# Performance work log

Hardware: AMD Instinct MI355X
Metric: run time of the kernel (lower is better)

Reference implementation:

```python
import jax, jax.numpy as jnp
import numpy as np

HEADS = 8
DIM_HEAD = 64

def setup_inputs() -> dict:
    key = jax.random.key(0)
    k1, k2 = jax.random.split(key)
    x = jax.random.normal(k1, (4, 2048, 512), dtype=jnp.float32)
    W_qkv = jax.random.normal(k2, (512, 3 * HEADS * DIM_HEAD), dtype=jnp.float32) * (512 ** -0.5)
    return {"x": x, "W_qkv": W_qkv}

def reference(x, W_qkv):
    b, n, _ = x.shape
    h, d = HEADS, DIM_HEAD
    scale = d ** -0.5
    qkv = x @ W_qkv                                   # [b, n, 3*h*d]
    q, k, v = jnp.split(qkv, 3, axis=-1)
    # 'b n (h d) -> b h n d'
    q = q.reshape(b, n, h, d).transpose(0, 2, 1, 3)
    k = k.reshape(b, n, h, d).transpose(0, 2, 1, 3)
    v = v.reshape(b, n, h, d).transpose(0, 2, 1, 3)
    scores = jnp.einsum('bhid,bhjd->bhij', q, k) * scale
    attn_w = jax.nn.softmax(scores, axis=-1)
    out = jnp.einsum('bhij,bhjd->bhid', attn_w, v)
    # 'b h i d -> b i (h d)'
    return out.transpose(0, 2, 1, 3).reshape(b, n, h * d)
```

## Files before the change

kernel.cpp:

```cpp
#include <hip/hip_runtime.h>

#define BATCH 4
#define NSEQ  2048
#define DMODEL 512
#define NHEAD 8
#define DHEAD 64
#define NQKV  1536

typedef __bf16 bf16x8 __attribute__((ext_vector_type(8)));
typedef __bf16 bf16x4 __attribute__((ext_vector_type(4)));
typedef float  f32x4  __attribute__((ext_vector_type(4)));
typedef short  s16x4  __attribute__((ext_vector_type(4)));

__device__ inline void async16(const __bf16* g, __bf16* l) {
    __builtin_amdgcn_global_load_lds(
        (const __attribute__((address_space(1))) void*)g,
        (__attribute__((address_space(3))) void*)l, 16, 0, 0);
}

__device__ inline bf16x8 cvt8(const float* __restrict__ p) {
    float4 a = *(const float4*)p;
    float4 b = *(const float4*)(p + 4);
    bf16x8 r;
    r[0] = (__bf16)a.x; r[1] = (__bf16)a.y; r[2] = (__bf16)a.z; r[3] = (__bf16)a.w;
    r[4] = (__bf16)b.x; r[5] = (__bf16)b.y; r[6] = (__bf16)b.z; r[7] = (__bf16)b.w;
    return r;
}

__device__ inline f32x4 mfma_pv(s16x4 a, s16x4 b, f32x4 c) {
#if !defined(__HIP_DEVICE_COMPILE__)
    (void)a; (void)b;
    return c;
#elif __has_builtin(__builtin_amdgcn_mfma_f32_16x16x16bf16_1k)
    return __builtin_amdgcn_mfma_f32_16x16x16bf16_1k(a, b, c, 0, 0, 0);
#else
    bf16x4 a4 = __builtin_bit_cast(bf16x4, a);
    bf16x4 b4 = __builtin_bit_cast(bf16x4, b);
    bf16x8 a8 = {}, b8 = {};
    for (int i = 0; i < 4; ++i) { a8[i] = a4[i]; b8[i] = b4[i]; }
    return __builtin_amdgcn_mfma_f32_16x16x32_bf16(a8, b8, c, 0, 0, 0);
#endif
}

#define QSCALE 0.18033688011112042f

__global__ __launch_bounds__(256) void prep_kernel(
    const float* __restrict__ W, __bf16* __restrict__ Wt,
    const float* __restrict__ x, __bf16* __restrict__ xb) {
    const int tid = threadIdx.x;
    const int bi = blockIdx.x;
    if (bi >= 192) {
        int g = ((bi - 192) * 256 + tid) * 8;
        bf16x8 r = cvt8(&x[g]);
        *(bf16x8*)&xb[g] = r;
        return;
    }
    __shared__ __bf16 t[64][65];
    const int n0 = (bi % 24) * 64, k0 = (bi / 24) * 64;
    const int cr = tid >> 4;
    const int cc = (tid & 15) * 4;
    for (int p = 0; p < 4; ++p) {
        int r = p * 16 + cr;
        float4 v = *(const float4*)&W[(size_t)(k0 + r) * NQKV + n0 + cc];
        t[r][cc + 0] = (__bf16)v.x; t[r][cc + 1] = (__bf16)v.y;
        t[r][cc + 2] = (__bf16)v.z; t[r][cc + 3] = (__bf16)v.w;
    }
    __syncthreads();
    for (int p = 0; p < 4; ++p) {
        int r = p * 16 + cr;
        bf16x4 o = {t[cc + 0][r], t[cc + 1][r], t[cc + 2][r], t[cc + 3][r]};
        *(bf16x4*)&Wt[(size_t)(n0 + r) * DMODEL + k0 + cc] = o;
    }
}

__global__ __launch_bounds__(512) void qkv_gemm_kernel(
    const __bf16* __restrict__ xb, const __bf16* __restrict__ Wt,
    __bf16* __restrict__ Qw, __bf16* __restrict__ Kw, __bf16* __restrict__ Vw) {
    __shared__ __align__(16) char smem[49152];
    __bf16* Al = (__bf16*)smem;
    __bf16* Bl = Al + 16384;
    __bf16* T  = (__bf16*)smem;

    const int tid  = threadIdx.x;
    const int w    = tid >> 6;
    const int lane = tid & 63;
    const int quad = lane >> 4;
    const int l15  = lane & 15;
    const int wm   = w >> 1, wn = w & 1;
    const int m0 = blockIdx.x * 256;
    const int n0 = blockIdx.y * 128;
    const int segrow = lane >> 3;
    const int sc = (lane & 7) ^ segrow;

    f32x4 acc[4][4];
    for (int i = 0; i < 4; ++i)
        for (int j = 0; j < 4; ++j)
            acc[i][j] = (f32x4){0.f, 0.f, 0.f, 0.f};

    for (int kt = 0; kt < 8; ++kt) {
        const int k0 = kt * 64;
        for (int i = 0; i < 2; ++i) {
            int seg = w * 2 + i;
            int row = seg * 8 + segrow;
            async16(&Wt[(size_t)(n0 + row) * DMODEL + k0 + sc * 8], &Bl[seg * 512]);
        }
        for (int i = 0; i < 4; ++i) {
            int seg = w * 4 + i;
            int row = seg * 8 + segrow;
            async16(&xb[(size_t)(m0 + row) * DMODEL + k0 + sc * 8], &Al[seg * 512]);
        }
        __syncthreads();
        for (int kc = 0; kc < 2; ++kc) {
            bf16x8 af[4], bfr[4];
            for (int mb = 0; mb < 4; ++mb) {
                int row = wm * 64 + mb * 16 + l15;
                af[mb] = *(const bf16x8*)&Al[(row >> 3) * 512 +
                    ((row & 7) * 8 + ((kc * 4 + quad) ^ (row & 7))) * 8];
            }
            for (int nb = 0; nb < 4; ++nb) {
                int row = wn * 64 + nb * 16 + l15;
                bfr[nb] = *(const bf16x8*)&Bl[row * 64 + (((kc * 4 + quad) ^ (l15 & 7)) * 8)];
            }
            for (int mb = 0; mb < 4; ++mb)
                for (int nb = 0; nb < 4; ++nb)
                    acc[mb][nb] = __builtin_amdgcn_mfma_f32_16x16x32_bf16(
                        af[mb], bfr[nb], acc[mb][nb], 0, 0, 0);
        }
        __syncthreads();
    }

    const int which = n0 >> 9;
    const int bb  = m0 >> 11;
    const int nq0 = m0 & 2047;

    for (int ph = 0; ph < 2; ++ph) {
        if (which <= 1) {
            if ((wm >> 1) == ph)
                for (int mb = 0; mb < 4; ++mb)
                    for (int nb = 0; nb < 4; ++nb)
                        for (int r = 0; r < 4; ++r) {
                            int ml = (wm & 1) * 64 + mb * 16 + quad * 4 + r;
                            int nl = wn * 64 + nb * 16 + l15;
                            float a = acc[mb][nb][r];
                            if (which == 0) a *= QSCALE;
                            T[ml * 136 + nl] = (__bf16)a;
                        }
            __syncthreads();
            __bf16* dst = which ? Kw : Qw;
            const int h0 = (n0 & 511) >> 6;
            const int region = tid >> 8;
            const int bh = bb * NHEAD + h0 + region;
            __bf16* base = dst + ((size_t)bh * NSEQ + nq0 + ph * 128) * DHEAD;
            for (int i = 0; i < 4; ++i) {
                int chunk = (tid & 255) + i * 256;
                int f = chunk * 8;
                int ml = f >> 6, dd = f & 63;
                bf16x8 v = *(const bf16x8*)&T[ml * 136 + region * 64 + dd];
                *(bf16x8*)&base[ml * 64 + dd] = v;
            }
        } else {
            if ((wm >> 1) == ph)
                for (int mb = 0; mb < 4; ++mb)
                    for (int nb = 0; nb < 4; ++nb) {
                        int nl = wn * 64 + nb * 16 + l15;
                        int mlb = (wm & 1) * 64 + mb * 16 + quad * 4;
                        bf16x4 v = {(__bf16)acc[mb][nb][0], (__bf16)acc[mb][nb][1],
                                    (__bf16)acc[mb][nb][2], (__bf16)acc[mb][nb][3]};
                        *(bf16x4*)&T[nl * 136 + mlb] = v;
                    }
            __syncthreads();
            const int hv0 = ((n0 - 1024) & 511) >> 6;
            for (int i = 0; i < 4; ++i) {
                int gc = i * 512 + tid;
                int row = gc >> 4, ch = gc & 15;
                bf16x8 v = *(const bf16x8*)&T[row * 136 + ch * 8];
                int bh = bb * NHEAD + hv0 + (row >> 6);
                int dd = row & 63;
                *(bf16x8*)&Vw[((size_t)bh * DHEAD + dd) * NSEQ + nq0 + ph * 128 + ch * 8] = v;
            }
        }
        __syncthreads();
    }
}

__global__ __launch_bounds__(512) void attn_kernel(
    const __bf16* __restrict__ Qw, const __bf16* __restrict__ Kw,
    const __bf16* __restrict__ Vw, float* __restrict__ out) {
    __shared__ __align__(16) char smem[65536];
    float* Of = (float*)smem;

    const int tid  = threadIdx.x;
    const int w    = tid >> 6;
    const int wg   = w & 3;
    const int half = w >> 2;
    const int lane = tid & 63;
    const int quad = lane >> 4;
    const int l15  = lane & 15;
    const int bh = blockIdx.y;
    const int bb = bh >> 3, h = bh & 7;
    const int q0 = blockIdx.x * 128 + wg * 32;
    const int segrow = lane >> 3;
    const int sc = (lane & 7) ^ segrow;

    __bf16* HB = (__bf16*)smem + half * 16384;

    const __bf16* Qh = Qw + (size_t)bh * NSEQ * DHEAD;
    const __bf16* Kh = Kw + (size_t)bh * NSEQ * DHEAD;
    const __bf16* Vh = Vw + (size_t)bh * DHEAD * NSEQ;

    bf16x8 qf[2][2];
#pragma unroll
    for (int qb = 0; qb < 2; ++qb)
#pragma unroll
        for (int kc = 0; kc < 2; ++kc)
            qf[qb][kc] = *(const bf16x8*)&Qh[(size_t)(q0 + qb * 16 + l15) * DHEAD + kc * 32 + quad * 8];

    int offk[2][4], offv[4][4];
#pragma unroll
    for (int kc = 0; kc < 2; ++kc)
#pragma unroll
        for (int kb = 0; kb < 4; ++kb)
            offk[kc][kb] = (kb * 16 + l15) * 64 + (((kc * 4 + quad) ^ (l15 & 7)) * 8);
#pragma unroll
    for (int kb = 0; kb < 4; ++kb)
#pragma unroll
        for (int db = 0; db < 4; ++db) {
            int d = db * 16 + l15;
            int g = kb * 2 + (quad >> 1);
            offv[kb][db] = (d >> 3) * 512 + (d & 7) * 64 +
                           ((g ^ (d & 7)) * 8) + (quad & 1) * 4;
        }

    const f32x4 fzero = (f32x4){0.f, 0.f, 0.f, 0.f};

    f32x4 O[4][2];
    float l_st[2] = {0.f, 0.f};
#pragma unroll
    for (int db = 0; db < 4; ++db)
#pragma unroll
        for (int qb = 0; qb < 2; ++qb)
            O[db][qb] = fzero;

    auto stage = [&](int it, int b) {
        const int k0 = (half * 16 + it) * 64;
        __bf16* KL = HB + b * 8192;
        __bf16* VL = KL + 4096;
        for (int i = 0; i < 2; ++i) {
            int seg = wg * 2 + i;
            int row = seg * 8 + segrow;
            async16(&Kh[(size_t)(k0 + row) * DHEAD + sc * 8], &KL[seg * 512]);
            async16(&Vh[(size_t)row * NSEQ + k0 + sc * 8], &VL[seg * 512]);
        }
    };

    stage(0, 0);
    for (int it = 0; it < 16; ++it) {
        __syncthreads();
        if (it < 15) stage(it + 1, (it + 1) & 1);
        const __bf16* Kb = HB + (it & 1) * 8192;
        const __bf16* Vb = Kb + 4096;

        f32x4 s[4][2];
#pragma unroll
        for (int kc = 0; kc < 2; ++kc) {
            bf16x8 ak[4];
#pragma unroll
            for (int kb = 0; kb < 4; ++kb)
                ak[kb] = *(const bf16x8*)&Kb[offk[kc][kb]];
#pragma unroll
            for (int kb = 0; kb < 4; ++kb)
#pragma unroll
                for (int qb = 0; qb < 2; ++qb)
                    s[kb][qb] = __builtin_amdgcn_mfma_f32_16x16x32_bf16(
                        ak[kb], qf[qb][kc], kc == 0 ? fzero : s[kb][qb], 0, 0, 0);
        }

        s16x4 pb[4][2];
#pragma unroll
        for (int qb = 0; qb < 2; ++qb) {
            float rsum = 0.f;
#pragma unroll
            for (int kb = 0; kb < 4; ++kb) {
                bf16x4 t;
#pragma unroll
                for (int r = 0; r < 4; ++r) {
                    float p = __builtin_amdgcn_exp2f(s[kb][qb][r]);
                    rsum += p;
                    t[r] = (__bf16)p;
                }
                pb[kb][qb] = __builtin_bit_cast(s16x4, t);
            }
            l_st[qb] += rsum;
        }

#pragma unroll
        for (int kb = 0; kb < 4; ++kb) {
            s16x4 av[4];
#pragma unroll
            for (int db = 0; db < 4; ++db)
                av[db] = *(const s16x4*)&Vb[offv[kb][db]];
#pragma unroll
            for (int db = 0; db < 4; ++db)
#pragma unroll
                for (int qb = 0; qb < 2; ++qb)
                    O[db][qb] = mfma_pv(av[db], pb[kb][qb], O[db][qb]);
        }
    }

    for (int qb = 0; qb < 2; ++qb) {
        l_st[qb] += __shfl_xor(l_st[qb], 16);
        l_st[qb] += __shfl_xor(l_st[qb], 32);
    }

    __syncthreads();
    if (half == 0) {
        for (int qb = 0; qb < 2; ++qb) {
            int q = wg * 32 + qb * 16 + l15;
            for (int db = 0; db < 4; ++db)
                *(f32x4*)&Of[q * 68 + db * 16 + quad * 4] = O[db][qb];
            if (quad == 0) Of[q * 68 + 64] = l_st[qb];
        }
    }
    __syncthreads();
    if (half == 1) {
        for (int qb = 0; qb < 2; ++qb) {
            int q = wg * 32 + qb * 16 + l15;
            float inv = 1.f / (l_st[qb] + Of[q * 68 + 64]);
            for (int db = 0; db < 4; ++db) {
                f32x4 v = *(const f32x4*)&Of[q * 68 + db * 16 + quad * 4];
                v = (v + O[db][qb]) * inv;
                *(f32x4*)&Of[q * 68 + db * 16 + quad * 4] = v;
            }
        }
    }
    __syncthreads();
    const int nqb = blockIdx.x * 128;
    for (int i = 0; i < 4; ++i) {
        int gc = i * 512 + tid;
        int row = gc >> 4, ch = gc & 15;
        f32x4 v = *(const f32x4*)&Of[row * 68 + ch * 4];
        *(f32x4*)&out[((size_t)(bb * NSEQ + nqb + row)) * DMODEL + h * DHEAD + ch * 4] = v;
    }
}

extern "C" void kernel_launch(void* const* d_in, const int* in_sizes, int n_in,
                              void* d_out, int out_size, void* d_ws, size_t ws_size,
                              hipStream_t stream) {
    const float* x = (const float*)d_in[0];
    const float* W = (const float*)d_in[1];
    float* out = (float*)d_out;

    __bf16* wsp = (__bf16*)d_ws;
    __bf16* Wt = wsp;
    __bf16* Qw = Wt + 786432;
    __bf16* Kw = Qw + 4194304;
    __bf16* Vw = Kw + 4194304;
    __bf16* xb = Vw + 4194304;

    prep_kernel<<<2240, 256, 0, stream>>>(W, Wt, x, xb);
    qkv_gemm_kernel<<<dim3(32, 12), 512, 0, stream>>>(xb, Wt, Qw, Kw, Vw);
    attn_kernel<<<dim3(16, 32), 512, 0, stream>>>(Qw, Kw, Vw, out);
}
```

Baseline: 132.9 us.

## Halve attention query tile and drop K/V double buffering to raise occupancy

The attention kernel now handles 64 queries per block instead of 128, with one 16-row query tile per wave. The grid doubles to 1024 blocks and shared memory is halved to 32KB by switching from double-buffered to single-buffered K/V staging, with a second barrier before each refill. Launch bounds request higher occupancy so more blocks can sit on each CU. In exchange, each K/V tile is reused by half as many queries, so global K/V traffic doubles, and the load of the next tile no longer overlaps with compute inside a block.

```diff
diff --git a/kernel.cpp b/kernel.cpp
--- a/kernel.cpp
+++ b/kernel.cpp
@@ -183,10 +183,10 @@
     }
 }
 
-__global__ __launch_bounds__(512) void attn_kernel(
+__global__ __launch_bounds__(512, 8) void attn_kernel(
     const __bf16* __restrict__ Qw, const __bf16* __restrict__ Kw,
     const __bf16* __restrict__ Vw, float* __restrict__ out) {
-    __shared__ __align__(16) char smem[65536];
+    __shared__ __align__(16) char smem[32768];
     float* Of = (float*)smem;
 
     const int tid  = threadIdx.x;
@@ -198,22 +198,20 @@
     const int l15  = lane & 15;
     const int bh = blockIdx.y;
     const int bb = bh >> 3, h = bh & 7;
-    const int q0 = blockIdx.x * 128 + wg * 32;
+    const int q0 = blockIdx.x * 64 + wg * 16;
     const int segrow = lane >> 3;
     const int sc = (lane & 7) ^ segrow;
 
-    __bf16* HB = (__bf16*)smem + half * 16384;
+    __bf16* HB = (__bf16*)smem + half * 8192;
 
     const __bf16* Qh = Qw + (size_t)bh * NSEQ * DHEAD;
     const __bf16* Kh = Kw + (size_t)bh * NSEQ * DHEAD;
     const __bf16* Vh = Vw + (size_t)bh * DHEAD * NSEQ;
 
-    bf16x8 qf[2][2];
-#pragma unroll
-    for (int qb = 0; qb < 2; ++qb)
-#pragma unroll
-        for (int kc = 0; kc < 2; ++kc)
-            qf[qb][kc] = *(const bf16x8*)&Qh[(size_t)(q0 + qb * 16 + l15) * DHEAD + kc * 32 + quad * 8];
+    bf16x8 qf[2];
+#pragma unroll
+    for (int kc = 0; kc < 2; ++kc)
+        qf[kc] = *(const bf16x8*)&Qh[(size_t)(q0 + l15) * DHEAD + kc * 32 + quad * 8];
 
     int offk[2][4], offv[4][4];
 #pragma unroll
@@ -233,18 +231,16 @@
 
     const f32x4 fzero = (f32x4){0.f, 0.f, 0.f, 0.f};
 
-    f32x4 O[4][2];
-    float l_st[2] = {0.f, 0.f};
+    f32x4 O[4];
+    float l_st = 0.f;
 #pragma unroll
     for (int db = 0; db < 4; ++db)
-#pragma unroll
-        for (int qb = 0; qb < 2; ++qb)
-            O[db][qb] = fzero;
-
-    auto stage = [&](int it, int b) {
+        O[db] = fzero;
+
+    auto stage = [&](int it) {
         const int k0 = (half * 16 + it) * 64;
-        __bf16* KL = HB + b * 8192;
-        __bf16* VL = KL + 4096;
+        __bf16* KL = HB;
+        __bf16* VL = HB + 4096;
         for (int i = 0; i < 2; ++i) {
             int seg = wg * 2 + i;
             int row = seg * 8 + segrow;
@@ -253,14 +249,13 @@
         }
     };
 
-    stage(0, 0);
+    stage(0);
     for (int it = 0; it < 16; ++it) {
         __syncthreads();
-        if (it < 15) stage(it + 1, (it + 1) & 1);
-        const __bf16* Kb = HB + (it & 1) * 8192;
-        const __bf16* Vb = Kb + 4096;
-
-        f32x4 s[4][2];
+        const __bf16* Kb = HB;
+        const __bf16* Vb = HB + 4096;
+
+        f32x4 s[4];
 #pragma unroll
         for (int kc = 0; kc < 2; ++kc) {
             bf16x8 ak[4];
@@ -269,28 +264,25 @@
                 ak[kb] = *(const bf16x8*)&Kb[offk[kc][kb]];
 #pragma unroll
             for (int kb = 0; kb < 4; ++kb)
-#pragma unroll
-                for (int qb = 0; qb < 2; ++qb)
-                    s[kb][qb] = __builtin_amdgcn_mfma_f32_16x16x32_bf16(
-                        ak[kb], qf[qb][kc], kc == 0 ? fzero : s[kb][qb], 0, 0, 0);
-        }
-
-        s16x4 pb[4][2];
-#pragma unroll
-        for (int qb = 0; qb < 2; ++qb) {
+                s[kb] = __builtin_amdgcn_mfma_f32_16x16x32_bf16(
+                    ak[kb], qf[kc], kc == 0 ? fzero : s[kb], 0, 0, 0);
+        }
+
+        s16x4 pb[4];
+        {
             float rsum = 0.f;
 #pragma unroll
             for (int kb = 0; kb < 4; ++kb) {
                 bf16x4 t;
 #pragma unroll
                 for (int r = 0; r < 4; ++r) {
-                    float p = __builtin_amdgcn_exp2f(s[kb][qb][r]);
+                    float p = __builtin_amdgcn_exp2f(s[kb][r]);
                     rsum += p;
                     t[r] = (__bf16)p;
                 }
-                pb[kb][qb] = __builtin_bit_cast(s16x4, t);
-            }
-            l_st[qb] += rsum;
+                pb[kb] = __builtin_bit_cast(s16x4, t);
+            }
+            l_st += rsum;
         }
 
 #pragma unroll
@@ -301,41 +293,37 @@
                 av[db] = *(const s16x4*)&Vb[offv[kb][db]];
 #pragma unroll
             for (int db = 0; db < 4; ++db)
-#pragma unroll
-                for (int qb = 0; qb < 2; ++qb)
-                    O[db][qb] = mfma_pv(av[db], pb[kb][qb], O[db][qb]);
-        }
-    }
-
-    for (int qb = 0; qb < 2; ++qb) {
-        l_st[qb] += __shfl_xor(l_st[qb], 16);
-        l_st[qb] += __shfl_xor(l_st[qb], 32);
-    }
+                O[db] = mfma_pv(av[db], pb[kb], O[db]);
+        }
+
+        if (it < 15) {
+            __syncthreads();
+            stage(it + 1);
+        }
+    }
+
+    l_st += __shfl_xor(l_st, 16);
+    l_st += __shfl_xor(l_st, 32);
 
     __syncthreads();
+    const int q = wg * 16 + l15;
     if (half == 0) {
-        for (int qb = 0; qb < 2; ++qb) {
-            int q = wg * 32 + qb * 16 + l15;
-            for (int db = 0; db < 4; ++db)
-                *(f32x4*)&Of[q * 68 + db * 16 + quad * 4] = O[db][qb];
-            if (quad == 0) Of[q * 68 + 64] = l_st[qb];
-        }
+        for (int db = 0; db < 4; ++db)
+            *(f32x4*)&Of[q * 68 + db * 16 + quad * 4] = O[db];
+        if (quad == 0) Of[q * 68 + 64] = l_st;
     }
     __syncthreads();
     if (half == 1) {
-        for (int qb = 0; qb < 2; ++qb) {
-            int q = wg * 32 + qb * 16 + l15;
-            float inv = 1.f / (l_st[qb] + Of[q * 68 + 64]);
-            for (int db = 0; db < 4; ++db) {
-                f32x4 v = *(const f32x4*)&Of[q * 68 + db * 16 + quad * 4];
-                v = (v + O[db][qb]) * inv;
-                *(f32x4*)&Of[q * 68 + db * 16 + quad * 4] = v;
-            }
+        float inv = 1.f / (l_st + Of[q * 68 + 64]);
+        for (int db = 0; db < 4; ++db) {
+            f32x4 v = *(const f32x4*)&Of[q * 68 + db * 16 + quad * 4];
+            v = (v + O[db]) * inv;
+            *(f32x4*)&Of[q * 68 + db * 16 + quad * 4] = v;
         }
     }
     __syncthreads();
-    const int nqb = blockIdx.x * 128;
-    for (int i = 0; i < 4; ++i) {
+    const int nqb = blockIdx.x * 64;
+    for (int i = 0; i < 2; ++i) {
         int gc = i * 512 + tid;
         int row = gc >> 4, ch = gc & 15;
         f32x4 v = *(const f32x4*)&Of[row * 68 + ch * 4];
@@ -359,5 +347,5 @@
 
     prep_kernel<<<2240, 256, 0, stream>>>(W, Wt, x, xb);
     qkv_gemm_kernel<<<dim3(32, 12), 512, 0, stream>>>(xb, Wt, Qw, Kw, Vw);
-    attn_kernel<<<dim3(16, 32), 512, 0, stream>>>(Qw, Kw, Vw, out);
-}
+    attn_kernel<<<dim3(32, 32), 512, 0, stream>>>(Qw, Kw, Vw, out);
+}
```

Measured after the change: 191.2 us. 43.9% more time.
